# Performance work log

Measured on AMD Instinct MI355X. Metric: run time of the kernel, lower is better.

## Reference

```python
import jax, jax.numpy as jnp
import numpy as np

C_Z = 128
C_S = 1024
C_S_OUT = 1024
B, L = 1, 1024


def setup_inputs() -> dict:
    key = jax.random.key(0)
    ks = jax.random.split(key, 8)
    s_z = jax.random.normal(ks[0], (B, L, L, C_Z), dtype=jnp.float32)
    s_s_in = jax.random.normal(ks[1], (B, L, C_S), dtype=jnp.float32)
    pair_mask = jnp.ones((B, L, L), dtype=jnp.float32)
    scale = 0.02
    return {
        "s_z": s_z,
        "s_s_in": s_s_in,
        "pair_mask": pair_mask,
        "ln_g": jnp.ones((C_Z,), jnp.float32),
        "ln_b": jnp.zeros((C_Z,), jnp.float32),
        "w1": jax.random.normal(ks[2], (C_Z, C_Z), jnp.float32) * scale,
        "b1": jnp.zeros((C_Z,), jnp.float32),
        "w2": jax.random.normal(ks[3], (C_Z, C_Z), jnp.float32) * scale,
        "b2": jnp.zeros((C_Z,), jnp.float32),
        "wc": jax.random.normal(ks[4], (C_S_OUT, 2 * C_Z + C_S), jnp.float32) * scale,
        "bc": jnp.zeros((C_S_OUT,), jnp.float32),
    }


def _layernorm(x, g, b, eps=1e-5):
    mu = jnp.mean(x, axis=-1, keepdims=True)
    var = jnp.mean(jnp.square(x - mu), axis=-1, keepdims=True)
    return (x - mu) * jax.lax.rsqrt(var + eps) * g + b


def reference(s_z, s_s_in, pair_mask, ln_g, ln_b, w1, b1, w2, b2, wc, bc):
    # LayerNorm -> Linear -> ReLU -> Linear over last dim (c_z)
    z = _layernorm(s_z, ln_g, ln_b)
    z = jax.nn.relu(jnp.einsum("blmc,dc->blmd", z, w1) + b1)
    z = jnp.einsum("blmc,dc->blmd", z, w2) + b2
    z = z * pair_mask[..., None]
    # masked mean over columns (dim=2) and rows (dim=1)
    norm_c = jnp.clip(jnp.sum(pair_mask, axis=2), 1.0, None)  # (B, L)
    s_s_c = jnp.sum(z, axis=2) / norm_c[..., None]            # (B, L, c_z)
    norm_r = jnp.clip(jnp.sum(pair_mask, axis=1), 1.0, None)
    s_s_r = jnp.sum(z, axis=1) / norm_r[..., None]
    cat = jnp.concatenate([s_s_c, s_s_r, s_s_in], axis=-1)    # (B, L, 2*c_z + c_s)
    return jnp.einsum("blc,dc->bld", cat, wc) + bc            # (B, L, c_s_out)
```

## Files before the change

kernel.cpp:

```cpp
#include <hip/hip_runtime.h>
#include <hip/hip_bf16.h>


typedef short bf16x8 __attribute__((ext_vector_type(8)));
typedef short short4v __attribute__((ext_vector_type(4)));
typedef float f32x16 __attribute__((ext_vector_type(16)));

static __device__ __forceinline__ short f2bf(float f) {
  unsigned u = __float_as_uint(f);
  u += 0x7fffu + ((u >> 16) & 1u);
  return (short)(u >> 16);
}
static __device__ __forceinline__ float bf2f(short s) {
  return __uint_as_float(((unsigned)(unsigned short)s) << 16);
}

__global__ __launch_bounds__(256, 2) void k_pair(
    const float* __restrict__ z, const float* __restrict__ pm,
    const float* __restrict__ lng, const float* __restrict__ lnb,
    const float* __restrict__ w1, const float* __restrict__ b1,
    float* __restrict__ gP, float* __restrict__ grP,
    float* __restrict__ Mc, float* __restrict__ Mr)
{
  __shared__ __align__(16) short As[2][64 * 136];
  __shared__ float maskS[2][64];

  const int tid  = threadIdx.x;
  const int lane = tid & 63;
  const int wv   = tid >> 6;
  const int rt   = wv >> 1;
  const int ch   = wv & 1;
  const int ln   = lane & 31;
  const int hh   = lane >> 5;
  const int bx   = blockIdx.x, by = blockIdx.y;
  const int l0   = by * 32;
  const int m0   = bx * 32;
  const int c8   = (tid & 15) * 8;

  float lg[8], lb[8];
  #pragma unroll
  for (int j = 0; j < 8; ++j) { lg[j] = lng[c8 + j]; lb[j] = lnb[c8 + j]; }

  float b1v[2];
  #pragma unroll
  for (int cc = 0; cc < 2; ++cc) b1v[cc] = b1[(ch * 2 + cc) * 32 + ln];

  bf16x8 bF[2][8];
  #pragma unroll
  for (int cc = 0; cc < 2; ++cc) {
    const int n = (ch * 2 + cc) * 32 + ln;
    #pragma unroll
    for (int k0 = 0; k0 < 8; ++k0) {
      const float* wp = w1 + n * 128 + k0 * 16 + hh * 8;
      float4 f0 = *(const float4*)wp;
      float4 f1 = *(const float4*)(wp + 4);
      bf16x8 t;
      t[0]=f2bf(f0.x); t[1]=f2bf(f0.y); t[2]=f2bf(f0.z); t[3]=f2bf(f0.w);
      t[4]=f2bf(f1.x); t[5]=f2bf(f1.y); t[6]=f2bf(f1.z); t[7]=f2bf(f1.w);
      bF[cc][k0] = t;
    }
  }

  float grA[2][16];
  #pragma unroll
  for (int cc = 0; cc < 2; ++cc)
    #pragma unroll
    for (int i = 0; i < 16; ++i) grA[cc][i] = 0.f;
  float mrAcc = 0.f;

  float4 xa[4], xb[4];
  float  mv = 0.f;
  auto LOADB = [&](int b) {
    #pragma unroll
    for (int p = 0; p < 4; ++p) {
      const int r = p * 16 + (tid >> 4);
      const int l = l0 + b * 2 + (r >> 5);
      const int m = m0 + (r & 31);
      const float* src = z + ((size_t)l * 1024 + (size_t)m) * 128 + c8;
      xa[p] = *(const float4*)src;
      xb[p] = *(const float4*)(src + 4);
    }
    if (tid < 64)
      mv = pm[(size_t)(l0 + b * 2 + (tid >> 5)) * 1024 + (m0 + (tid & 31))];
  };

  LOADB(0);

  #pragma unroll 1
  for (int b = 0; b < 16; ++b) {
    const int buf = b & 1;
    #pragma unroll
    for (int p = 0; p < 4; ++p) {
      const int r = p * 16 + (tid >> 4);
      float x[8] = {xa[p].x, xa[p].y, xa[p].z, xa[p].w,
                    xb[p].x, xb[p].y, xb[p].z, xb[p].w};
      float s = 0.f, s2 = 0.f;
      #pragma unroll
      for (int j = 0; j < 8; ++j) { s += x[j]; s2 += x[j] * x[j]; }
      #pragma unroll
      for (int off = 1; off < 16; off <<= 1) {
        s  += __shfl_xor(s, off);
        s2 += __shfl_xor(s2, off);
      }
      const float mu  = s * (1.f / 128.f);
      const float var = s2 * (1.f / 128.f) - mu * mu;
      const float rs  = rsqrtf(var + 1e-5f);
      bf16x8 o;
      #pragma unroll
      for (int j = 0; j < 8; ++j) o[j] = f2bf((x[j] - mu) * rs * lg[j] + lb[j]);
      *(bf16x8*)(&As[buf][r * 136 + c8]) = o;
    }
    if (tid < 64) maskS[buf][tid] = mv;
    __syncthreads();

    if (b < 15) LOADB(b + 1);

    f32x16 acc0, acc1;
    #pragma unroll
    for (int i = 0; i < 16; ++i) { acc0[i] = 0.f; acc1[i] = 0.f; }
    #pragma unroll
    for (int k0 = 0; k0 < 8; ++k0) {
      bf16x8 aF = *(bf16x8*)(&As[buf][(rt * 32 + ln) * 136 + k0 * 16 + hh * 8]);
      acc0 = __builtin_amdgcn_mfma_f32_32x32x16_bf16(aF, bF[0][k0], acc0, 0, 0, 0);
      acc1 = __builtin_amdgcn_mfma_f32_32x32x16_bf16(aF, bF[1][k0], acc1, 0, 0, 0);
    }

    float mrow[16];
    #pragma unroll
    for (int i = 0; i < 16; ++i) {
      const int cr = (i & 3) + 8 * (i >> 2) + 4 * hh;
      mrow[i] = maskS[buf][rt * 32 + cr];
    }
    const int lrow = l0 + b * 2 + rt;
    float s0 = 0.f, s1 = 0.f;
    #pragma unroll
    for (int i = 0; i < 16; ++i) {
      const float v0 = fmaxf(acc0[i] + b1v[0], 0.f) * mrow[i];
      const float v1 = fmaxf(acc1[i] + b1v[1], 0.f) * mrow[i];
      grA[0][i] += v0; grA[1][i] += v1;
      s0 += v0; s1 += v1;
    }
    s0 += __shfl_xor(s0, 32);
    s1 += __shfl_xor(s1, 32);
    if (lane < 32) {
      float* dst = gP + ((size_t)bx * 1024 + lrow) * 128;
      dst[(ch * 2 + 0) * 32 + lane] = s0;
      dst[(ch * 2 + 1) * 32 + lane] = s1;
    }

    if (wv == 0) {
      const float v = maskS[buf][lane];
      mrAcc += v;
      float rsum = v;
      #pragma unroll
      for (int off = 1; off < 32; off <<= 1) rsum += __shfl_xor(rsum, off);
      if (ln == 0) atomicAdd(&Mc[l0 + b * 2 + hh], rsum);
    }
  }

  if (wv == 0) {
    const float v = mrAcc + __shfl_xor(mrAcc, 32);
    if (lane < 32) atomicAdd(&Mr[m0 + lane], v);
  }

  __syncthreads();
  float* red1 = (float*)&As[0][0];
  if (rt == 1) {
    #pragma unroll
    for (int cc = 0; cc < 2; ++cc)
      #pragma unroll
      for (int i = 0; i < 16; ++i) {
        const int cr = (i & 3) + 8 * (i >> 2) + 4 * hh;
        red1[((ch * 2 + cc) * 32 + cr) * 32 + ln] = grA[cc][i];
      }
  }
  __syncthreads();
  if (rt == 0) {
    #pragma unroll
    for (int cc = 0; cc < 2; ++cc)
      #pragma unroll
      for (int i = 0; i < 16; ++i) {
        const int cr = (i & 3) + 8 * (i >> 2) + 4 * hh;
        const float v = grA[cc][i] + red1[((ch * 2 + cc) * 32 + cr) * 32 + ln];
        grP[((size_t)by * 1024 + (m0 + cr)) * 128 + (ch * 2 + cc) * 32 + ln] = v;
      }
  }
}

__global__ void k_reduce(const float* __restrict__ gP, const float* __restrict__ grP,
                         float* __restrict__ g, float* __restrict__ gr)
{
  const int idx = blockIdx.x * 256 + threadIdx.x;
  const bool isG = idx < 32768;
  const int t = isG ? idx : idx - 32768;
  const float* src = isG ? gP : grP;
  float* dst = isG ? g : gr;
  const int row = t >> 5;
  const int c4  = (t & 31) * 4;
  float4 s = {0.f, 0.f, 0.f, 0.f};
  #pragma unroll 8
  for (int x = 0; x < 32; ++x) {
    float4 v = *(const float4*)(src + ((size_t)x * 1024 + row) * 128 + c4);
    s.x += v.x; s.y += v.y; s.z += v.z; s.w += v.w;
  }
  *(float4*)(dst + (size_t)row * 128 + c4) = s;
}

__global__ __launch_bounds__(256, 2) void k_seqproj(
    const float* __restrict__ gg, const float* __restrict__ w2,
    const float* __restrict__ b2, const float* __restrict__ Mc,
    const float* __restrict__ Mr, short* __restrict__ Ah, short* __restrict__ Al)
{
  __shared__ __align__(16) short As[64 * 136];
  __shared__ float Mvs[64];

  const int tid = threadIdx.x, lane = tid & 63, wv = tid >> 6;
  const int rt = wv >> 1, ch = wv & 1, ln = lane & 31, hh = lane >> 5;
  const int r0 = blockIdx.x * 64;
  const int c8 = (tid & 15) * 8;

  float b2v[2];
  #pragma unroll
  for (int cc = 0; cc < 2; ++cc) b2v[cc] = b2[(ch * 2 + cc) * 32 + ln];

  bf16x8 bF[2][8];
  #pragma unroll
  for (int cc = 0; cc < 2; ++cc) {
    const int n = (ch * 2 + cc) * 32 + ln;
    #pragma unroll
    for (int k0 = 0; k0 < 8; ++k0) {
      const float* wp = w2 + n * 128 + k0 * 16 + hh * 8;
      float4 f0 = *(const float4*)wp;
      float4 f1 = *(const float4*)(wp + 4);
      bf16x8 t;
      t[0]=f2bf(f0.x); t[1]=f2bf(f0.y); t[2]=f2bf(f0.z); t[3]=f2bf(f0.w);
      t[4]=f2bf(f1.x); t[5]=f2bf(f1.y); t[6]=f2bf(f1.z); t[7]=f2bf(f1.w);
      bF[cc][k0] = t;
    }
  }

  #pragma unroll
  for (int p = 0; p < 4; ++p) {
    const int r = p * 16 + (tid >> 4);
    const float* src = gg + (size_t)(r0 + r) * 128 + c8;
    float4 f0 = *(const float4*)src;
    float4 f1 = *(const float4*)(src + 4);
    bf16x8 o;
    o[0]=f2bf(f0.x); o[1]=f2bf(f0.y); o[2]=f2bf(f0.z); o[3]=f2bf(f0.w);
    o[4]=f2bf(f1.x); o[5]=f2bf(f1.y); o[6]=f2bf(f1.z); o[7]=f2bf(f1.w);
    *(bf16x8*)(&As[r * 136 + c8]) = o;
  }
  if (tid < 64) {
    const int p = r0 + tid;
    Mvs[tid] = (p < 1024) ? Mc[p] : Mr[p - 1024];
  }
  __syncthreads();

  f32x16 acc0, acc1;
  #pragma unroll
  for (int i = 0; i < 16; ++i) { acc0[i] = 0.f; acc1[i] = 0.f; }
  #pragma unroll
  for (int k0 = 0; k0 < 8; ++k0) {
    bf16x8 aF = *(bf16x8*)(&As[(rt * 32 + ln) * 136 + k0 * 16 + hh * 8]);
    acc0 = __builtin_amdgcn_mfma_f32_32x32x16_bf16(aF, bF[0][k0], acc0, 0, 0, 0);
    acc1 = __builtin_amdgcn_mfma_f32_32x32x16_bf16(aF, bF[1][k0], acc1, 0, 0, 0);
  }

  const int base = (r0 < 1024) ? 0 : 128;
  #pragma unroll
  for (int i = 0; i < 16; ++i) {
    const int cr = (i & 3) + 8 * (i >> 2) + 4 * hh;
    const int p = r0 + rt * 32 + cr;
    const int row = p & 1023;
    const float mvv = Mvs[rt * 32 + cr];
    const float dn = fmaxf(mvv, 1.f);
    const float v0 = (acc0[i] + b2v[0] * mvv) / dn;
    const float v1 = (acc1[i] + b2v[1] * mvv) / dn;
    const int c0 = base + (ch * 2 + 0) * 32 + ln;
    const int c1 = base + (ch * 2 + 1) * 32 + ln;
    const short h0 = f2bf(v0), h1 = f2bf(v1);
    Ah[(size_t)row * 1280 + c0] = h0;
    Al[(size_t)row * 1280 + c0] = f2bf(v0 - bf2f(h0));
    Ah[(size_t)row * 1280 + c1] = h1;
    Al[(size_t)row * 1280 + c1] = f2bf(v1 - bf2f(h1));
  }
}

__global__ void k_split(const float* __restrict__ s_in, const float* __restrict__ wc,
                        short* __restrict__ Ah, short* __restrict__ Al,
                        short* __restrict__ Bh, short* __restrict__ Bl)
{
  const int idx = blockIdx.x * 256 + threadIdx.x;

  if (idx < 262144) {
    const int row = idx >> 8;
    const int c4  = (idx & 255) * 4;
    float4 v = *(const float4*)(s_in + (size_t)row * 1024 + c4);
    float x[4] = {v.x, v.y, v.z, v.w};
    short4v hi, lo;
    #pragma unroll
    for (int j = 0; j < 4; ++j) {
      const short h = f2bf(x[j]);
      hi[j] = h; lo[j] = f2bf(x[j] - bf2f(h));
    }
    const size_t o = (size_t)row * 1280 + 256 + c4;
    *(short4v*)(Ah + o) = hi;
    *(short4v*)(Al + o) = lo;
  }
  if (idx < 327680) {
    const int row = idx / 320;
    const int c4  = (idx - row * 320) * 4;
    float4 v = *(const float4*)(wc + (size_t)row * 1280 + c4);
    float x[4] = {v.x, v.y, v.z, v.w};
    short4v hi, lo;
    #pragma unroll
    for (int j = 0; j < 4; ++j) {
      const short h = f2bf(x[j]);
      hi[j] = h; lo[j] = f2bf(x[j] - bf2f(h));
    }
    const size_t o = (size_t)row * 1280 + c4;
    *(short4v*)(Bh + o) = hi;
    *(short4v*)(Bl + o) = lo;
  }
}

__global__ __launch_bounds__(256, 2) void k_final(
    const short* __restrict__ Ah, const short* __restrict__ Al,
    const short* __restrict__ Bh, const short* __restrict__ Bl,
    const float* __restrict__ bc, float* __restrict__ out)
{
  __shared__ __align__(16) short sAh[64 * 40], sAl[64 * 40];
  __shared__ __align__(16) short sBh[64 * 40], sBl[64 * 40];
  const int tid = threadIdx.x, lane = tid & 63, wv = tid >> 6;
  const int mi = (wv >> 1) * 32, ni = (wv & 1) * 32;
  const int ln = lane & 31, hh = lane >> 5;
  const int m0 = blockIdx.y * 64, n0 = blockIdx.x * 64;
  const int rS = tid >> 2;
  const int kb = (tid & 3) * 8;

  const float bcv = bc[n0 + ni + ln];
  f32x16 acc;
  #pragma unroll
  for (int i = 0; i < 16; ++i) acc[i] = 0.f;

  bf16x8 rAh, rAl, rBh, rBl;
  auto LOADK = [&](int kk0) {
    rAh = *(const bf16x8*)(Ah + (size_t)(m0 + rS) * 1280 + kk0 + kb);
    rAl = *(const bf16x8*)(Al + (size_t)(m0 + rS) * 1280 + kk0 + kb);
    rBh = *(const bf16x8*)(Bh + (size_t)(n0 + rS) * 1280 + kk0 + kb);
    rBl = *(const bf16x8*)(Bl + (size_t)(n0 + rS) * 1280 + kk0 + kb);
  };
  LOADK(0);

  #pragma unroll 1
  for (int kk0 = 0; kk0 < 1280; kk0 += 32) {
    if (kk0) __syncthreads();
    *(bf16x8*)(sAh + rS * 40 + kb) = rAh;
    *(bf16x8*)(sAl + rS * 40 + kb) = rAl;
    *(bf16x8*)(sBh + rS * 40 + kb) = rBh;
    *(bf16x8*)(sBl + rS * 40 + kb) = rBl;
    __syncthreads();
    if (kk0 < 1280 - 32) LOADK(kk0 + 32);

    #pragma unroll
    for (int k0 = 0; k0 < 2; ++k0) {
      bf16x8 aH = *(bf16x8*)(sAh + (mi + ln) * 40 + k0 * 16 + hh * 8);
      bf16x8 aL = *(bf16x8*)(sAl + (mi + ln) * 40 + k0 * 16 + hh * 8);
      bf16x8 bH = *(bf16x8*)(sBh + (ni + ln) * 40 + k0 * 16 + hh * 8);
      bf16x8 bL = *(bf16x8*)(sBl + (ni + ln) * 40 + k0 * 16 + hh * 8);
      acc = __builtin_amdgcn_mfma_f32_32x32x16_bf16(aH, bH, acc, 0, 0, 0);
      acc = __builtin_amdgcn_mfma_f32_32x32x16_bf16(aH, bL, acc, 0, 0, 0);
      acc = __builtin_amdgcn_mfma_f32_32x32x16_bf16(aL, bH, acc, 0, 0, 0);
    }
  }

  #pragma unroll
  for (int i = 0; i < 16; ++i) {
    const int cr = (i & 3) + 8 * (i >> 2) + 4 * hh;
    out[(size_t)(m0 + mi + cr) * 1024 + n0 + ni + ln] = acc[i] + bcv;
  }
}

extern "C" void kernel_launch(void* const* d_in, const int* in_sizes, int n_in,
                              void* d_out, int out_size, void* d_ws, size_t ws_size,
                              hipStream_t stream) {
  const float* s_z    = (const float*)d_in[0];
  const float* s_s_in = (const float*)d_in[1];
  const float* pmask  = (const float*)d_in[2];
  const float* ln_g   = (const float*)d_in[3];
  const float* ln_b   = (const float*)d_in[4];
  const float* w1     = (const float*)d_in[5];
  const float* b1     = (const float*)d_in[6];
  const float* w2     = (const float*)d_in[7];
  const float* b2     = (const float*)d_in[8];
  const float* wc     = (const float*)d_in[9];
  const float* bc     = (const float*)d_in[10];
  float* outp = (float*)d_out;

  float* Mc  = (float*)d_ws;
  float* Mr  = Mc + 1024;
  float* g   = Mr + 1024;
  float* gr  = g  + 131072;
  float* gP  = gr + 131072;
  float* grP = gP + 4194304;
  short* Ah  = (short*)(grP + 4194304);
  short* Al  = Ah + (size_t)1024 * 1280;
  short* Bh  = Al + (size_t)1024 * 1280;
  short* Bl  = Bh + (size_t)1024 * 1280;

  hipMemsetAsync(d_ws, 0, 2048 * sizeof(float), stream);

  k_split<<<1280, 256, 0, stream>>>(s_s_in, wc, Ah, Al, Bh, Bl);
  k_pair<<<dim3(32, 32), 256, 0, stream>>>(s_z, pmask, ln_g, ln_b, w1, b1, gP, grP, Mc, Mr);
  k_reduce<<<256, 256, 0, stream>>>(gP, grP, g, gr);
  k_seqproj<<<32, 256, 0, stream>>>(g, w2, b2, Mc, Mr, Ah, Al);
  k_final<<<dim3(16, 16), 256, 0, stream>>>(Ah, Al, Bh, Bl, bc, outp);
}
```

Measured before the change: 771.9 us.

## Fold LayerNorm affine into W1 and double threads per pair block

```diff
diff --git a/kernel.cpp b/kernel.cpp
--- a/kernel.cpp
+++ b/kernel.cpp
@@ -15,7 +15,7 @@
   return __uint_as_float(((unsigned)(unsigned short)s) << 16);
 }
 
-__global__ __launch_bounds__(256, 2) void k_pair(
+__global__ __launch_bounds__(512, 4) void k_pair(
     const float* __restrict__ z, const float* __restrict__ pm,
     const float* __restrict__ lng, const float* __restrict__ lnb,
     const float* __restrict__ w1, const float* __restrict__ b1,
@@ -23,57 +23,62 @@
     float* __restrict__ Mc, float* __restrict__ Mr)
 {
   __shared__ __align__(16) short As[2][64 * 136];
-  __shared__ float maskS[2][64];
+  __shared__ __align__(16) float rowdat[2][64][4];
 
   const int tid  = threadIdx.x;
   const int lane = tid & 63;
   const int wv   = tid >> 6;
-  const int rt   = wv >> 1;
-  const int ch   = wv & 1;
+  const int rt   = wv >> 2;
+  const int cq   = wv & 3;
   const int ln   = lane & 31;
   const int hh   = lane >> 5;
   const int bx   = blockIdx.x, by = blockIdx.y;
   const int l0   = by * 32;
   const int m0   = bx * 32;
   const int c8   = (tid & 15) * 8;
-
-  float lg[8], lb[8];
-  #pragma unroll
-  for (int j = 0; j < 8; ++j) { lg[j] = lng[c8 + j]; lb[j] = lnb[c8 + j]; }
-
-  float b1v[2];
-  #pragma unroll
-  for (int cc = 0; cc < 2; ++cc) b1v[cc] = b1[(ch * 2 + cc) * 32 + ln];
-
-  bf16x8 bF[2][8];
-  #pragma unroll
-  for (int cc = 0; cc < 2; ++cc) {
-    const int n = (ch * 2 + cc) * 32 + ln;
-    #pragma unroll
-    for (int k0 = 0; k0 < 8; ++k0) {
-      const float* wp = w1 + n * 128 + k0 * 16 + hh * 8;
-      float4 f0 = *(const float4*)wp;
-      float4 f1 = *(const float4*)(wp + 4);
-      bf16x8 t;
-      t[0]=f2bf(f0.x); t[1]=f2bf(f0.y); t[2]=f2bf(f0.z); t[3]=f2bf(f0.w);
-      t[4]=f2bf(f1.x); t[5]=f2bf(f1.y); t[6]=f2bf(f1.z); t[7]=f2bf(f1.w);
-      bF[cc][k0] = t;
-    }
-  }
-
-  float grA[2][16];
-  #pragma unroll
-  for (int cc = 0; cc < 2; ++cc)
-    #pragma unroll
-    for (int i = 0; i < 16; ++i) grA[cc][i] = 0.f;
+  const int rstage = tid >> 4;
+
+  const int dcol = cq * 32 + ln;
+  float uacc = 0.f, wacc = 0.f;
+  bf16x8 bF[8];
+  #pragma unroll
+  for (int k0 = 0; k0 < 8; ++k0) {
+    const int kb = k0 * 16 + hh * 8;
+    const float* wp = w1 + dcol * 128 + kb;
+    float4 f0 = *(const float4*)wp;
+    float4 f1 = *(const float4*)(wp + 4);
+    float4 g0 = *(const float4*)(lng + kb);
+    float4 g1 = *(const float4*)(lng + kb + 4);
+    float4 e0 = *(const float4*)(lnb + kb);
+    float4 e1 = *(const float4*)(lnb + kb + 4);
+    float wr[8] = {f0.x, f0.y, f0.z, f0.w, f1.x, f1.y, f1.z, f1.w};
+    float gg[8] = {g0.x, g0.y, g0.z, g0.w, g1.x, g1.y, g1.z, g1.w};
+    float be[8] = {e0.x, e0.y, e0.z, e0.w, e1.x, e1.y, e1.z, e1.w};
+    bf16x8 t;
+    #pragma unroll
+    for (int j = 0; j < 8; ++j) {
+      t[j] = f2bf(wr[j] * gg[j]);
+      uacc += bf2f(t[j]);
+      wacc += wr[j] * be[j];
+    }
+    bF[k0] = t;
+  }
+  uacc += __shfl_xor(uacc, 32);
+  wacc += __shfl_xor(wacc, 32);
+  const float u_d  = uacc;
+  const float wb_d = wacc + b1[dcol];
+
+  float grA[16];
+  #pragma unroll
+  for (int i = 0; i < 16; ++i) grA[i] = 0.f;
   float mrAcc = 0.f;
 
-  float4 xa[4], xb[4];
+  float4 xa[2], xb[2];
   float  mv = 0.f;
   auto LOADB = [&](int b) {
     #pragma unroll
-    for (int p = 0; p < 4; ++p) {
-      const int r = p * 16 + (tid >> 4);
+    for (int p = 0; p < 2; ++p) {
+      const int r = p * 32 + rstage;
       const int l = l0 + b * 2 + (r >> 5);
       const int m = m0 + (r & 31);
       const float* src = z + ((size_t)l * 1024 + (size_t)m) * 128 + c8;
@@ -90,13 +95,13 @@
   for (int b = 0; b < 16; ++b) {
     const int buf = b & 1;
     #pragma unroll
-    for (int p = 0; p < 4; ++p) {
-      const int r = p * 16 + (tid >> 4);
+    for (int p = 0; p < 2; ++p) {
+      const int r = p * 32 + rstage;
       float x[8] = {xa[p].x, xa[p].y, xa[p].z, xa[p].w,
                     xb[p].x, xb[p].y, xb[p].z, xb[p].w};
       float s = 0.f, s2 = 0.f;
       #pragma unroll
-      for (int j = 0; j < 8; ++j) { s += x[j]; s2 += x[j] * x[j]; }
+      for (int j = 0; j < 8; ++j) { s += x[j]; s2 = fmaf(x[j], x[j], s2); }
       #pragma unroll
       for (int off = 1; off < 16; off <<= 1) {
         s  += __shfl_xor(s, off);
@@ -107,49 +112,43 @@
       const float rs  = rsqrtf(var + 1e-5f);
       bf16x8 o;
       #pragma unroll
-      for (int j = 0; j < 8; ++j) o[j] = f2bf((x[j] - mu) * rs * lg[j] + lb[j]);
+      for (int j = 0; j < 8; ++j) o[j] = f2bf(x[j]);
       *(bf16x8*)(&As[buf][r * 136 + c8]) = o;
-    }
-    if (tid < 64) maskS[buf][tid] = mv;
+      if ((tid & 15) == 0) {
+        rowdat[buf][r][0] = rs;
+        rowdat[buf][r][1] = rs * mu;
+      }
+    }
+    if (tid < 64) rowdat[buf][tid][2] = mv;
     __syncthreads();
 
     if (b < 15) LOADB(b + 1);
 
-    f32x16 acc0, acc1;
-    #pragma unroll
-    for (int i = 0; i < 16; ++i) { acc0[i] = 0.f; acc1[i] = 0.f; }
+    f32x16 acc;
+    #pragma unroll
+    for (int i = 0; i < 16; ++i) acc[i] = 0.f;
     #pragma unroll
     for (int k0 = 0; k0 < 8; ++k0) {
       bf16x8 aF = *(bf16x8*)(&As[buf][(rt * 32 + ln) * 136 + k0 * 16 + hh * 8]);
-      acc0 = __builtin_amdgcn_mfma_f32_32x32x16_bf16(aF, bF[0][k0], acc0, 0, 0, 0);
-      acc1 = __builtin_amdgcn_mfma_f32_32x32x16_bf16(aF, bF[1][k0], acc1, 0, 0, 0);
-    }
-
-    float mrow[16];
+      acc = __builtin_amdgcn_mfma_f32_32x32x16_bf16(aF, bF[k0], acc, 0, 0, 0);
+    }
+
+    const int lrow = l0 + b * 2 + rt;
+    float s = 0.f;
     #pragma unroll
     for (int i = 0; i < 16; ++i) {
       const int cr = (i & 3) + 8 * (i >> 2) + 4 * hh;
-      mrow[i] = maskS[buf][rt * 32 + cr];
-    }
-    const int lrow = l0 + b * 2 + rt;
-    float s0 = 0.f, s1 = 0.f;
-    #pragma unroll
-    for (int i = 0; i < 16; ++i) {
-      const float v0 = fmaxf(acc0[i] + b1v[0], 0.f) * mrow[i];
-      const float v1 = fmaxf(acc1[i] + b1v[1], 0.f) * mrow[i];
-      grA[0][i] += v0; grA[1][i] += v1;
-      s0 += v0; s1 += v1;
-    }
-    s0 += __shfl_xor(s0, 32);
-    s1 += __shfl_xor(s1, 32);
-    if (lane < 32) {
-      float* dst = gP + ((size_t)bx * 1024 + lrow) * 128;
-      dst[(ch * 2 + 0) * 32 + lane] = s0;
-      dst[(ch * 2 + 1) * 32 + lane] = s1;
-    }
+      const float4 rd = *(const float4*)&rowdat[buf][rt * 32 + cr][0];
+      const float h = fmaf(rd.x, acc[i], fmaf(-rd.y, u_d, wb_d));
+      const float v = fmaxf(h, 0.f) * rd.z;
+      grA[i] += v; s += v;
+    }
+    s += __shfl_xor(s, 32);
+    if (lane < 32)
+      gP[((size_t)bx * 1024 + lrow) * 128 + cq * 32 + lane] = s;
 
     if (wv == 0) {
-      const float v = maskS[buf][lane];
+      const float v = rowdat[buf][lane][2];
       mrAcc += v;
       float rsum = v;
       #pragma unroll
@@ -164,26 +163,22 @@
   }
 
   __syncthreads();
-  float* red1 = (float*)&As[0][0];
+  float* red = (float*)&As[0][0];
   if (rt == 1) {
     #pragma unroll
-    for (int cc = 0; cc < 2; ++cc)
-      #pragma unroll
-      for (int i = 0; i < 16; ++i) {
-        const int cr = (i & 3) + 8 * (i >> 2) + 4 * hh;
-        red1[((ch * 2 + cc) * 32 + cr) * 32 + ln] = grA[cc][i];
-      }
+    for (int i = 0; i < 16; ++i) {
+      const int cr = (i & 3) + 8 * (i >> 2) + 4 * hh;
+      red[(cq * 32 + cr) * 32 + ln] = grA[i];
+    }
   }
   __syncthreads();
   if (rt == 0) {
     #pragma unroll
-    for (int cc = 0; cc < 2; ++cc)
-      #pragma unroll
-      for (int i = 0; i < 16; ++i) {
-        const int cr = (i & 3) + 8 * (i >> 2) + 4 * hh;
-        const float v = grA[cc][i] + red1[((ch * 2 + cc) * 32 + cr) * 32 + ln];
-        grP[((size_t)by * 1024 + (m0 + cr)) * 128 + (ch * 2 + cc) * 32 + ln] = v;
-      }
+    for (int i = 0; i < 16; ++i) {
+      const int cr = (i & 3) + 8 * (i >> 2) + 4 * hh;
+      const float v = grA[i] + red[(cq * 32 + cr) * 32 + ln];
+      grP[((size_t)by * 1024 + (m0 + cr)) * 128 + cq * 32 + ln] = v;
+    }
   }
 }
 
@@ -411,7 +406,7 @@
   hipMemsetAsync(d_ws, 0, 2048 * sizeof(float), stream);
 
   k_split<<<1280, 256, 0, stream>>>(s_s_in, wc, Ah, Al, Bh, Bl);
-  k_pair<<<dim3(32, 32), 256, 0, stream>>>(s_z, pmask, ln_g, ln_b, w1, b1, gP, grP, Mc, Mr);
+  k_pair<<<dim3(32, 32), 512, 0, stream>>>(s_z, pmask, ln_g, ln_b, w1, b1, gP, grP, Mc, Mr);
   k_reduce<<<256, 256, 0, stream>>>(gP, grP, g, gr);
   k_seqproj<<<32, 256, 0, stream>>>(g, w2, b2, Mc, Mr, Ah, Al);
   k_final<<<dim3(16, 16), 256, 0, stream>>>(Ah, Al, Bh, Bl, bc, outp);
```

Result: no change. 785.1 us (+1.7%).
